# Kernel tuning notes

Hardware: AMD Instinct MI355X
Metric: run time of the kernel (lower is better)

Reference implementation:

```python
import jax, jax.numpy as jnp
import numpy as np

B, S, D, O = 8, 2048, 4096, 4096
E, R = 8, 16
LORA_ALPHA = 32
SCALING = LORA_ALPHA / R  # 2.0
IMG_START, IMG_LEN = 34, 576


def setup_inputs() -> dict:
    key = jax.random.key(0)
    ks = jax.random.split(key, 7)
    x = jax.random.normal(ks[0], (B, S, D), dtype=jnp.float32)
    W = jax.random.normal(ks[1], (O, D), dtype=jnp.float32) * 0.02   # frozen original linear weight
    b = jnp.zeros((O,), dtype=jnp.float32)                            # original linear bias
    A = jax.random.normal(ks[2], (E, R, D), dtype=jnp.float32) * 0.02  # stacked lora_A per expert
    Bm = jax.random.normal(ks[3], (E, O, R), dtype=jnp.float32) * 0.02
    Wr = jax.random.normal(ks[4], (E, D), dtype=jnp.float32) * 0.02   # router weight
    br = jnp.zeros((E,), dtype=jnp.float32)                           # router bias
    return {"x": x, "W": W, "b": b, "A": A, "Bm": Bm, "Wr": Wr, "br": br}


def reference(x, W, b, A, Bm, Wr, br):
    # original_module applied to all tokens (torch applies it piecewise to the
    # three slices with the same frozen Linear -> identical to one full matmul)
    orig = jnp.einsum('bsd,od->bso', x, W) + b                 # [B,S,O]

    x_img = x[:, IMG_START:IMG_START + IMG_LEN]                # [B,576,D]
    logits = jnp.einsum('bsd,ed->bse', x_img, Wr) + br         # [B,576,E]
    routing = jax.nn.softmax(logits, axis=-1)

    # top-1 hard routing (argmax -> one-hot); straight-through estimator output
    idx = jnp.argmax(routing, axis=-1)                         # [B,576] int
    onehot = jax.nn.one_hot(idx, E, dtype=x.dtype)             # [B,576,E]
    expert_choice = onehot - jax.lax.stop_gradient(routing) + routing

    # sparse per-expert LoRA dispatch, expressed as masked grouped matmuls:
    # t[b,s,e,r] = x_img @ A_e^T ; mask by one-hot so only the selected
    # expert contributes, then contract with B_e -> identical math to the
    # torch gather/matmul/scatter loop (with dropout in eval mode).
    t = jnp.einsum('bsd,erd->bser', x_img, A)                  # [B,576,E,R]
    t = t * onehot[:, :, :, None]
    lora = jnp.einsum('bser,eor->bso', t, Bm) * SCALING        # [B,576,O]

    final = orig.at[:, IMG_START:IMG_START + IMG_LEN].add(lora)
    return final, routing, expert_choice
```

## Files before the change

### kernel.cpp

```cpp
#include <hip/hip_runtime.h>
#include <cstdint>
#include <cstddef>

#define Bq 8
#define Sq 2048
#define Dq 4096
#define Oq 4096
#define Eq 8
#define Rq 16
#define IMG_START 34
#define IMG_LEN 576
#define SCALING 2.0f

#define M_TOT (Bq * Sq)
#define FINAL_N ((size_t)M_TOT * Oq)
#define ROUT_OFF FINAL_N
#define EC_OFF (FINAL_N + (size_t)Bq * IMG_LEN * Eq)

typedef short bf16x8 __attribute__((ext_vector_type(8)));
typedef float f32x4 __attribute__((ext_vector_type(4)));

__device__ __forceinline__ unsigned short f2bf(float f) {
    unsigned int u = __float_as_uint(f);
    unsigned int lsb = (u >> 16) & 1u;
    u += 0x7fffu + lsb;
    return (unsigned short)(u >> 16);
}

__device__ __forceinline__ void gload16(const void* g, void* l) {
    __builtin_amdgcn_global_load_lds(
        (const __attribute__((address_space(1))) void*)g,
        (__attribute__((address_space(3))) void*)l, 16, 0, 0);
}

__global__ __launch_bounds__(256) void cvt_kernel(const float* __restrict__ in,
                                                  unsigned short* __restrict__ out,
                                                  long n4) {
    long i = (long)blockIdx.x * blockDim.x + threadIdx.x;
    long stride = (long)gridDim.x * blockDim.x;
    typedef unsigned short us4 __attribute__((ext_vector_type(4)));
    for (long v = i; v < n4; v += stride) {
        float4 f = ((const float4*)in)[v];
        us4 o;
        o.x = f2bf(f.x); o.y = f2bf(f.y); o.z = f2bf(f.z); o.w = f2bf(f.w);
        ((us4*)out)[v] = o;
    }
}

#define BM 128
#define BN 128
#define BK 64

__global__ __launch_bounds__(256, 3) void gemm_bt(
    const unsigned short* __restrict__ A,
    const unsigned short* __restrict__ Bt,
    const float* __restrict__ bias,
    float* __restrict__ C) {
    const int Mn = M_TOT, Nn = Oq, Kn = Dq;

    __shared__ __align__(16) unsigned short As[BM * BK];
    __shared__ __align__(16) unsigned short Bs[BN * BK];

    int tid = threadIdx.x;
    int lane = tid & 63;
    int wid = tid >> 6;

    int nbn = Nn / BN;
    int nwg = (Mn / BM) * nbn;
    int cpx = nwg >> 3;
    int bid = blockIdx.x;
    int swz = (bid & 7) * cpx + (bid >> 3);
    int tm = swz / nbn, tn = swz % nbn;

    int wr = wid >> 1, wc = wid & 1;
    int lr = lane & 15;
    int lk = (lane >> 4) * 8;

    f32x4 acc[4][4] = {};

    const size_t arow0 = (size_t)tm * BM;
    const size_t brow0 = (size_t)tn * BN;

    for (int kt = 0; kt < Kn; kt += BK) {
#pragma unroll
        for (int i = 0; i < 4; ++i) {
            int chunk = i * 256 + tid;
            int row = chunk >> 3, c8 = chunk & 7;
            gload16(A + (arow0 + row) * Kn + kt + c8 * 8,
                    &As[(size_t)(i * 256 + (wid << 6)) * 8]);
        }
#pragma unroll
        for (int i = 0; i < 4; ++i) {
            int chunk = i * 256 + tid;
            int row = chunk >> 3, c8 = chunk & 7;
            gload16(Bt + (brow0 + row) * Kn + kt + c8 * 8,
                    &Bs[(size_t)(i * 256 + (wid << 6)) * 8]);
        }
        __syncthreads();

#pragma unroll
        for (int kk = 0; kk < BK; kk += 32) {
            bf16x8 af[4], bf[4];
#pragma unroll
            for (int mi = 0; mi < 4; ++mi)
                af[mi] = *(const bf16x8*)&As[(wr * 64 + mi * 16 + lr) * BK + kk + lk];
#pragma unroll
            for (int ni = 0; ni < 4; ++ni)
                bf[ni] = *(const bf16x8*)&Bs[(wc * 64 + ni * 16 + lr) * BK + kk + lk];
#pragma unroll
            for (int mi = 0; mi < 4; ++mi)
#pragma unroll
                for (int ni = 0; ni < 4; ++ni)
                    acc[mi][ni] = __builtin_amdgcn_mfma_f32_16x16x32_bf16(
                        af[mi], bf[ni], acc[mi][ni], 0, 0, 0);
        }
        __syncthreads();
    }

#pragma unroll
    for (int ni = 0; ni < 4; ++ni) {
        int col = tn * BN + wc * 64 + ni * 16 + lr;
        float bv = bias[col];
#pragma unroll
        for (int mi = 0; mi < 4; ++mi) {
            int row0 = tm * BM + wr * 64 + mi * 16 + ((lane >> 4) << 2);
            f32x4 v = acc[mi][ni];
#pragma unroll
            for (int r = 0; r < 4; ++r)
                C[(size_t)(row0 + r) * Nn + col] = v[r] + bv;
        }
    }
}

__global__ __launch_bounds__(256) void route_lora(
    const float* __restrict__ x,
    const float* __restrict__ A,
    const float* __restrict__ Bm,
    const float* __restrict__ Wr,
    const float* __restrict__ br,
    float* __restrict__ out) {
    int token = blockIdx.x;
    int bb = token / IMG_LEN, si = token - bb * IMG_LEN;
    int s = IMG_START + si;
    const float* xrow = x + ((size_t)bb * Sq + s) * Dq;

    __shared__ __align__(16) float xs[Dq];
    __shared__ double lg[Eq];
    __shared__ float tv[Rq];
    __shared__ int esel;

    int tid = threadIdx.x, lane = tid & 63, wid = tid >> 6;

    for (int i = tid; i < Dq / 4; i += 256)
        ((float4*)xs)[i] = ((const float4*)xrow)[i];
    __syncthreads();

#pragma unroll
    for (int eo = 0; eo < 2; ++eo) {
        int e = wid * 2 + eo;
        const float* wre = Wr + (size_t)e * Dq;
        double sum = 0.0;
        for (int k = lane; k < Dq; k += 64)
            sum += (double)xs[k] * (double)wre[k];
        for (int off = 32; off; off >>= 1) sum += __shfl_xor(sum, off);
        if (lane == 0) lg[e] = sum + (double)br[e];
    }
    __syncthreads();

    if (tid == 0) {
        double mx = lg[0]; int am = 0;
        for (int e = 1; e < Eq; ++e) if (lg[e] > mx) { mx = lg[e]; am = e; }
        double ex[Eq], den = 0.0;
        for (int e = 0; e < Eq; ++e) { ex[e] = exp(lg[e] - mx); den += ex[e]; }
        for (int e = 0; e < Eq; ++e) {
            float rf = (float)(ex[e] / den);
            out[ROUT_OFF + (size_t)token * Eq + e] = rf;
            float oh = (e == am) ? 1.0f : 0.0f;
            out[EC_OFF + (size_t)token * Eq + e] = (oh - rf) + rf;
        }
        esel = am;
    }
    __syncthreads();
    int e = esel;

#pragma unroll
    for (int ro = 0; ro < 4; ++ro) {
        int r = wid * 4 + ro;
        const float* ar = A + ((size_t)e * Rq + r) * Dq;
        float sum = 0.0f;
        for (int k = lane; k < Dq; k += 64) sum += xs[k] * ar[k];
        for (int off = 32; off; off >>= 1) sum += __shfl_xor(sum, off);
        if (lane == 0) tv[r] = sum;
    }
    __syncthreads();

    float* orow = out + ((size_t)bb * Sq + s) * Oq;
    for (int o = tid; o < Oq; o += 256) {
        const float4* bp = (const float4*)(Bm + ((size_t)e * Oq + o) * Rq);
        float acc = 0.0f;
#pragma unroll
        for (int j = 0; j < 4; ++j) {
            float4 bv = bp[j];
            acc += bv.x * tv[j * 4 + 0] + bv.y * tv[j * 4 + 1] +
                   bv.z * tv[j * 4 + 2] + bv.w * tv[j * 4 + 3];
        }
        orow[o] += SCALING * acc;
    }
}

extern "C" void kernel_launch(void* const* d_in, const int* in_sizes, int n_in,
                              void* d_out, int out_size, void* d_ws, size_t ws_size,
                              hipStream_t stream) {
    const float* x  = (const float*)d_in[0];
    const float* W  = (const float*)d_in[1];
    const float* b  = (const float*)d_in[2];
    const float* A  = (const float*)d_in[3];
    const float* Bm = (const float*)d_in[4];
    const float* Wr = (const float*)d_in[5];
    const float* br = (const float*)d_in[6];
    float* out = (float*)d_out;

    unsigned short* xb = (unsigned short*)d_ws;
    unsigned short* Wb = xb + (size_t)M_TOT * Dq;

    cvt_kernel<<<2048, 256, 0, stream>>>(x, xb, (long)M_TOT * Dq / 4);
    cvt_kernel<<<1024, 256, 0, stream>>>(W, Wb, (long)Oq * Dq / 4);

    gemm_bt<<<(M_TOT / BM) * (Oq / BN), 256, 0, stream>>>(xb, Wb, b, out);

    route_lora<<<Bq * IMG_LEN, 256, 0, stream>>>(x, A, Bm, Wr, br, out);
}
```

Baseline: 1.735 ms.

## Replace GEMM with 256x256 double-buffered, swizzled-LDS, phase-pipelined MFMA kernel

Replaces the 128x128 single-buffered bf16 GEMM with a 256x256-tile, 512-thread kernel. It double-buffers LDS in quarter-tile chunks and interleaves async global-to-LDS loads with MFMA phases, using explicit barriers, vmcnt waits and setprio. It also XOR-swizzles the LDS layout to avoid bank conflicts. The aim is to hide memory latency and raise data reuse per tile. The cost is much more register and LDS pressure and fragile hand-written synchronisation.

```diff
diff --git a/kernel.cpp b/kernel.cpp
--- a/kernel.cpp
+++ b/kernel.cpp
@@ -16,6 +16,8 @@
 #define FINAL_N ((size_t)M_TOT * Oq)
 #define ROUT_OFF FINAL_N
 #define EC_OFF (FINAL_N + (size_t)Bq * IMG_LEN * Eq)
+
+#define NT 64
 
 typedef short bf16x8 __attribute__((ext_vector_type(8)));
 typedef float f32x4 __attribute__((ext_vector_type(4)));
@@ -47,89 +49,117 @@
     }
 }
 
-#define BM 128
-#define BN 128
-#define BK 64
-
-__global__ __launch_bounds__(256, 3) void gemm_bt(
-    const unsigned short* __restrict__ A,
-    const unsigned short* __restrict__ Bt,
+
+__global__ __launch_bounds__(512, 2) void gemm256(
+    const unsigned short* __restrict__ Ag,
+    const unsigned short* __restrict__ Bg,
     const float* __restrict__ bias,
     float* __restrict__ C) {
-    const int Mn = M_TOT, Nn = Oq, Kn = Dq;
-
-    __shared__ __align__(16) unsigned short As[BM * BK];
-    __shared__ __align__(16) unsigned short Bs[BN * BK];
-
-    int tid = threadIdx.x;
-    int lane = tid & 63;
-    int wid = tid >> 6;
-
-    int nbn = Nn / BN;
-    int nwg = (Mn / BM) * nbn;
-    int cpx = nwg >> 3;
+    __shared__ __align__(16) unsigned short ldsA[2][2][8192];
+    __shared__ __align__(16) unsigned short ldsB[2][2][8192];
+
+    const int tid = threadIdx.x;
+    const int lane = tid & 63, wid = tid >> 6;
+    const int wr = wid >> 2, wc = wid & 3;
+    const int lr = lane & 15, hi = lane >> 4, l7 = lane & 7;
+
     int bid = blockIdx.x;
-    int swz = (bid & 7) * cpx + (bid >> 3);
-    int tm = swz / nbn, tn = swz % nbn;
-
-    int wr = wid >> 1, wc = wid & 1;
-    int lr = lane & 15;
-    int lk = (lane >> 4) * 8;
-
-    f32x4 acc[4][4] = {};
-
-    const size_t arow0 = (size_t)tm * BM;
-    const size_t brow0 = (size_t)tn * BN;
-
-    for (int kt = 0; kt < Kn; kt += BK) {
-#pragma unroll
-        for (int i = 0; i < 4; ++i) {
-            int chunk = i * 256 + tid;
-            int row = chunk >> 3, c8 = chunk & 7;
-            gload16(A + (arow0 + row) * Kn + kt + c8 * 8,
-                    &As[(size_t)(i * 256 + (wid << 6)) * 8]);
+    int swz = (bid & 7) * 128 + (bid >> 3);
+    int tm = swz >> 4, tn = swz & 15;
+    const size_t mrow0 = (size_t)tm * 256, nrow0 = (size_t)tn * 256;
+
+    const int q0 = tid, q1 = 512 + tid;
+    const int r0 = q0 >> 3, c0 = (q0 & 7) ^ (r0 & 7);
+    const int r1 = q1 >> 3, c1 = (q1 & 7) ^ (r1 & 7);
+    const size_t garow0 = (mrow0 + (size_t)((r0 >> 6) << 7) + (r0 & 63)) * Dq + c0 * 8;
+    const size_t garow1 = (mrow0 + (size_t)((r1 >> 6) << 7) + (r1 & 63)) * Dq + c1 * 8;
+    const size_t gbrow0 = (nrow0 + (size_t)((r0 >> 5) << 6) + (r0 & 31)) * Dq + c0 * 8;
+    const size_t gbrow1 = (nrow0 + (size_t)((r1 >> 5) << 6) + (r1 & 31)) * Dq + c1 * 8;
+    const int ldst0 = (0 * 512 + (wid << 6)) * 8;
+    const int ldst1 = (1 * 512 + (wid << 6)) * 8;
+
+    const int sl0 = (hi ^ l7) * 8;
+    const int sl1 = ((4 + hi) ^ l7) * 8;
+    const int arow = wr * 4096 + lr * 64;
+    const int brow = wc * 2048 + lr * 64;
+
+    f32x4 acc[8][4] = {};
+
+#define STAGE_A(bf, mh, tile) do {                                              \
+        int kt_ = ((tile) < NT ? (tile) : NT - 1) * 64;                         \
+        gload16(Ag + garow0 + (size_t)(mh) * 64 * Dq + kt_, &ldsA[bf][mh][ldst0]); \
+        gload16(Ag + garow1 + (size_t)(mh) * 64 * Dq + kt_, &ldsA[bf][mh][ldst1]); \
+    } while (0)
+#define STAGE_B(bf, nh, tile) do {                                              \
+        int kt_ = ((tile) < NT ? (tile) : NT - 1) * 64;                         \
+        gload16(Bg + gbrow0 + (size_t)(nh) * 32 * Dq + kt_, &ldsB[bf][nh][ldst0]); \
+        gload16(Bg + gbrow1 + (size_t)(nh) * 32 * Dq + kt_, &ldsB[bf][nh][ldst1]); \
+    } while (0)
+
+#define PHASE(bf, mh, nh, STAGES, WAITC) do {                                   \
+        bf16x8 a0[4], a1[4], b0[2], b1[2];                                      \
+        _Pragma("unroll") for (int mi = 0; mi < 4; ++mi) {                      \
+            a0[mi] = *(const bf16x8*)&ldsA[bf][mh][arow + mi * 1024 + sl0];     \
+            a1[mi] = *(const bf16x8*)&ldsA[bf][mh][arow + mi * 1024 + sl1];     \
+        }                                                                       \
+        _Pragma("unroll") for (int ni = 0; ni < 2; ++ni) {                      \
+            b0[ni] = *(const bf16x8*)&ldsB[bf][nh][brow + ni * 1024 + sl0];     \
+            b1[ni] = *(const bf16x8*)&ldsB[bf][nh][brow + ni * 1024 + sl1];     \
+        }                                                                       \
+        STAGES                                                                  \
+        asm volatile("s_barrier" ::: "memory");                                 \
+        asm volatile("s_waitcnt lgkmcnt(0)" ::: "memory");                      \
+        __builtin_amdgcn_sched_barrier(0);                                      \
+        __builtin_amdgcn_s_setprio(1);                                          \
+        _Pragma("unroll") for (int mi = 0; mi < 4; ++mi)                        \
+            _Pragma("unroll") for (int ni = 0; ni < 2; ++ni) {                  \
+                acc[(mh) * 4 + mi][(nh) * 2 + ni] =                             \
+                    __builtin_amdgcn_mfma_f32_16x16x32_bf16(                    \
+                        a0[mi], b0[ni], acc[(mh) * 4 + mi][(nh) * 2 + ni], 0, 0, 0); \
+                acc[(mh) * 4 + mi][(nh) * 2 + ni] =                             \
+                    __builtin_amdgcn_mfma_f32_16x16x32_bf16(                    \
+                        a1[mi], b1[ni], acc[(mh) * 4 + mi][(nh) * 2 + ni], 0, 0, 0); \
+            }                                                                   \
+        __builtin_amdgcn_s_setprio(0);                                          \
+        WAITC                                                                   \
+        asm volatile("s_barrier" ::: "memory");                                 \
+    } while (0)
+
+    STAGE_A(0, 0, 0); STAGE_B(0, 0, 0); STAGE_B(0, 1, 0); STAGE_A(0, 1, 0);
+    STAGE_A(1, 0, 1); STAGE_B(1, 0, 1);
+    asm volatile("s_waitcnt vmcnt(4)" ::: "memory");
+    asm volatile("s_barrier" ::: "memory");
+
+    for (int j = 0; j < 32; ++j) {
+        int t1 = 2 * j + 1;
+        PHASE(0, 0, 0, { STAGE_B(1, 1, t1); STAGE_A(1, 1, t1); }, );
+        PHASE(0, 0, 1, , );
+        PHASE(0, 1, 0, { STAGE_A(0, 0, t1 + 1); }, );
+        PHASE(0, 1, 1, { STAGE_B(0, 0, t1 + 1); },
+              asm volatile("s_waitcnt vmcnt(4)" ::: "memory"); );
+        PHASE(1, 0, 0, { STAGE_B(0, 1, t1 + 1); }, );
+        PHASE(1, 0, 1, { STAGE_A(0, 1, t1 + 1); }, );
+        PHASE(1, 1, 0, { STAGE_A(1, 0, t1 + 2); }, );
+        PHASE(1, 1, 1, { STAGE_B(1, 0, t1 + 2); },
+              asm volatile("s_waitcnt vmcnt(4)" ::: "memory"); );
+    }
+
+#pragma unroll
+    for (int bi = 0; bi < 4; ++bi) {
+        int col = (int)nrow0 + wc * 64 + (bi >> 1) * 32 + (bi & 1) * 16 + lr;
+        float bv = bias[col];
+#pragma unroll
+        for (int ai = 0; ai < 8; ++ai) {
+            int row0 = (int)mrow0 + wr * 128 + (ai >> 2) * 64 + (ai & 3) * 16 + hi * 4;
+            f32x4 v = acc[ai][bi];
+#pragma unroll
+            for (int r = 0; r < 4; ++r)
+                C[(size_t)(row0 + r) * Oq + col] = v[r] + bv;
         }
-#pragma unroll
-        for (int i = 0; i < 4; ++i) {
-            int chunk = i * 256 + tid;
-            int row = chunk >> 3, c8 = chunk & 7;
-            gload16(Bt + (brow0 + row) * Kn + kt + c8 * 8,
-                    &Bs[(size_t)(i * 256 + (wid << 6)) * 8]);
-        }
-        __syncthreads();
-
-#pragma unroll
-        for (int kk = 0; kk < BK; kk += 32) {
-            bf16x8 af[4], bf[4];
-#pragma unroll
-            for (int mi = 0; mi < 4; ++mi)
-                af[mi] = *(const bf16x8*)&As[(wr * 64 + mi * 16 + lr) * BK + kk + lk];
-#pragma unroll
-            for (int ni = 0; ni < 4; ++ni)
-                bf[ni] = *(const bf16x8*)&Bs[(wc * 64 + ni * 16 + lr) * BK + kk + lk];
-#pragma unroll
-            for (int mi = 0; mi < 4; ++mi)
-#pragma unroll
-                for (int ni = 0; ni < 4; ++ni)
-                    acc[mi][ni] = __builtin_amdgcn_mfma_f32_16x16x32_bf16(
-                        af[mi], bf[ni], acc[mi][ni], 0, 0, 0);
-        }
-        __syncthreads();
-    }
-
-#pragma unroll
-    for (int ni = 0; ni < 4; ++ni) {
-        int col = tn * BN + wc * 64 + ni * 16 + lr;
-        float bv = bias[col];
-#pragma unroll
-        for (int mi = 0; mi < 4; ++mi) {
-            int row0 = tm * BM + wr * 64 + mi * 16 + ((lane >> 4) << 2);
-            f32x4 v = acc[mi][ni];
-#pragma unroll
-            for (int r = 0; r < 4; ++r)
-                C[(size_t)(row0 + r) * Nn + col] = v[r] + bv;
-        }
-    }
+    }
+#undef STAGE_A
+#undef STAGE_B
+#undef PHASE
 }
 
 __global__ __launch_bounds__(256) void route_lora(
@@ -226,7 +256,7 @@
     cvt_kernel<<<2048, 256, 0, stream>>>(x, xb, (long)M_TOT * Dq / 4);
     cvt_kernel<<<1024, 256, 0, stream>>>(W, Wb, (long)Oq * Dq / 4);
 
-    gemm_bt<<<(M_TOT / BM) * (Oq / BN), 256, 0, stream>>>(xb, Wb, b, out);
+    gemm256<<<(M_TOT / 256) * (Oq / 256), 512, 0, stream>>>(xb, Wb, b, out);
 
     route_lora<<<Bq * IMG_LEN, 256, 0, stream>>>(x, A, Bm, Wr, br, out);
 }
```

Result: faster. 1.660 ms (-4.3%).
